# Performance work log

Hardware: AMD Instinct MI355X
Metric: run time of the kernel (lower is better)

Reference implementation:

```python
import jax, jax.numpy as jnp
import numpy as np

NEG_SLOPE = 0.1
BN_EPS = 1e-5

def lrelu(z):
    return jax.nn.leaky_relu(z, NEG_SLOPE)

def conv1d(x, w, b):
    # x: [B,C,L], w: [O,I,K], 'same' padding for K=3
    y = jax.lax.conv_general_dilated(x, w, (1,), [(1, 1)], dimension_numbers=('NCH', 'OIH', 'NCH'))
    return y + b[None, :, None]

def batchnorm_train(x, g, be):
    # training-mode BatchNorm1d over (B, L) per channel; x: [B,C,L]
    m = x.mean(axis=(0, 2), keepdims=True)
    v = x.var(axis=(0, 2), keepdims=True)
    return g[None, :, None] * (x - m) * jax.lax.rsqrt(v + BN_EPS) + be[None, :, None]

def setup_inputs() -> dict:
    key = jax.random.key(0)
    ks = jax.random.split(key, 16)
    L, B, E = 100, 32, 512
    F, K, M, H, DEC = 256, 3, 128, 512, 512
    D = F + 2  # cnn feats + 2 coord dims
    s = 0.02
    inp = {
        'x': jax.random.normal(ks[0], (L, B, E), jnp.float32),
        'h': jax.random.normal(ks[1], (B, H), jnp.float32),
        'cw1': jax.random.normal(ks[2], (F, E, K), jnp.float32) * s,
        'cb1': jnp.zeros((F,), jnp.float32),
        'g1': jnp.ones((F,), jnp.float32), 'be1': jnp.zeros((F,), jnp.float32),
        'cw2': jax.random.normal(ks[3], (F, F, K), jnp.float32) * s,
        'cb2': jnp.zeros((F,), jnp.float32),
        'g2': jnp.ones((F,), jnp.float32), 'be2': jnp.zeros((F,), jnp.float32),
        'cw3': jax.random.normal(ks[4], (F, F, K), jnp.float32) * s,
        'cb3': jnp.zeros((F,), jnp.float32),
        'g3': jnp.ones((F,), jnp.float32), 'be3': jnp.zeros((F,), jnp.float32),
        'cw4': jax.random.normal(ks[5], (F, F, K), jnp.float32) * s,
        'cb4': jnp.zeros((F,), jnp.float32),
        'g4': jnp.ones((F,), jnp.float32), 'be4': jnp.zeros((F,), jnp.float32),
        'W1': jax.random.normal(ks[6], (2 * D + H, M), jnp.float32) * s,
        'b1': jnp.zeros((M,), jnp.float32),
        'W2': jax.random.normal(ks[7], (M, M), jnp.float32) * s,
        'b2': jnp.zeros((M,), jnp.float32),
        'W3': jax.random.normal(ks[8], (M, M), jnp.float32) * s,
        'b3': jnp.zeros((M,), jnp.float32),
        'W4': jax.random.normal(ks[9], (M, M), jnp.float32) * s,
        'b4': jnp.zeros((M,), jnp.float32),
        'F1': jax.random.normal(ks[10], (M, M), jnp.float32) * s,
        'fb1': jnp.zeros((M,), jnp.float32),
        'F2': jax.random.normal(ks[11], (M, DEC), jnp.float32) * s,
        'fb2': jnp.zeros((DEC,), jnp.float32),
    }
    return inp

def reference(x, h, cw1, cb1, g1, be1, cw2, cb2, g2, be2, cw3, cb3, g3, be3,
              cw4, cb4, g4, be4, W1, b1, W2, b2, W3, b3, W4, b4, F1, fb1, F2, fb2):
    # x: [L,B,E] -> [B,E,L]
    xc = jnp.transpose(x, (1, 2, 0))
    for cw, cb, g, be in ((cw1, cb1, g1, be1), (cw2, cb2, g2, be2),
                          (cw3, cb3, g3, be3), (cw4, cb4, g4, be4)):
        xc = batchnorm_train(lrelu(conv1d(xc, cw, cb)), g, be)
    xc = jnp.transpose(xc, (0, 2, 1))  # [B,L,F]
    B, L, _ = xc.shape
    # coordinate tensor: cvt_coord(i, L) = [(i/sqrt(L)-2)/2, (i%sqrt(L)-2)/2]
    i = jnp.arange(L, dtype=jnp.float32)
    sL = jnp.sqrt(jnp.float32(L))
    coord = jnp.stack([(i / sL - 2.0) / 2.0, (jnp.mod(i, sL) - 2.0) / 2.0], axis=-1)
    xf = jnp.concatenate([xc, jnp.broadcast_to(coord, (B, L, 2))], axis=-1)  # [B,L,D]
    D = xf.shape[-1]
    # pair[b,i,j] = [xf[b,j], xf[b,i], h[b]]; split W1 to avoid materializing concat
    Wa, Wb, Wc = W1[:D], W1[D:2 * D], W1[2 * D:]
    A = xf @ Wa                              # contribution of x_j, [B,L,M]
    C = xf @ Wb + (h @ Wc + b1)[:, None, :]  # contribution of x_i and h, [B,L,M]
    g = lrelu(C[:, :, None, :] + A[:, None, :, :])  # [B,L,L,M]
    g = lrelu(g @ W2 + b2)
    g = lrelu(g @ W3 + b3)
    g = lrelu(g @ W4 + b4)
    s = g.sum(axis=(1, 2))  # sum-pool over all L*L pairs -> [B,M]
    out = lrelu(lrelu(s @ F1 + fb1) @ F2 + fb2)  # [B,dec_hid]
    return out
```

## Files before the change

kernel.cpp:

```cpp
#include <hip/hip_runtime.h>
#include <hip/hip_bf16.h>
#include <stdint.h>
#include <stddef.h>

#define NEG 0.1f

typedef __attribute__((ext_vector_type(8))) short short8;
typedef __attribute__((ext_vector_type(16))) float floatx16;

__device__ __forceinline__ unsigned f2bf(float f) {
  union { float f; unsigned u; } v; v.f = f;
  unsigned r = v.u + 0x7FFFu + ((v.u >> 16) & 1u);
  return r >> 16;
}
__device__ __forceinline__ unsigned pk2bf(float a, float b) {
  __hip_bfloat162 hh = __float22bfloat162_rn(make_float2(a, b));
  union { __hip_bfloat162 h; unsigned u; } v; v.h = hh; return v.u;
}
__device__ __forceinline__ float bits2f(unsigned u) {
  union { unsigned u; float f; } v; v.u = u; return v.f;
}


__global__ void k_prep(const float* __restrict__ cw1, const float* __restrict__ cw2,
                       const float* __restrict__ cw3, const float* __restrict__ cw4,
                       unsigned short* __restrict__ wt1, unsigned short* __restrict__ wt2,
                       unsigned short* __restrict__ wt3, unsigned short* __restrict__ wt4,
                       const float* __restrict__ W1, unsigned short* __restrict__ wabf,
                       const float* __restrict__ W2, const float* __restrict__ W3,
                       const float* __restrict__ W4, unsigned short* __restrict__ wmlp,
                       const float* __restrict__ h, float* __restrict__ hc,
                       float* __restrict__ zmem) {
  __shared__ float tile[256];
  int bid = blockIdx.x, tid = threadIdx.x;
  if (bid < 1280) {
    int z = bid;
    int E; const float* cw; unsigned short* wt;
    if (z < 512) { E = 512; cw = cw1; wt = wt1; }
    else {
      int q = (z - 512) >> 8; E = 256;
      cw = (q == 0) ? cw2 : ((q == 1) ? cw3 : cw4);
      wt = (q == 0) ? wt2 : ((q == 1) ? wt3 : wt4);
      z = (z - 512) & 255;
    }
    int NCw = (3 * E) >> 6;
    int idx = z * 256 + tid;
    int f = idx / E, e = idx - f * E;
    const float* s = cw + (size_t)idx * 3;
    int ct = f >> 5, i32 = f & 31;
#pragma unroll
    for (int ks = 0; ks < 3; ++ks) {
      int kcol = ks * E + e;
      int cg = kcol >> 6, kk = (kcol >> 4) & 3, hh = (kcol >> 3) & 1, j = kcol & 7;
      wt[(size_t)((((ct * NCw + cg) * 4 + kk) * 2 + hh) * 32 + i32) * 8 + j] =
          (unsigned short)f2bf(s[ks]);
    }
  } else if (bid < 1304) {
    int tw = bid - 1280;
    int half = tw / 12, rem = tw % 12, dt = rem >> 1, nt = rem & 1;
    int c = tid & 63, rq = tid >> 6;
    int n = half * 128 + nt * 64 + c;
    int ct = n >> 5, i32 = n & 31;
#pragma unroll
    for (int it = 0; it < 16; ++it) {
      int r2 = rq + it * 4;
      int kp = dt * 64 + r2;
      if (kp < 320) {
        float v = (kp < 258) ? W1[(size_t)(half * 258 + kp) * 128 + nt * 64 + c] : 0.f;
        int cg = kp >> 6, kk = (kp >> 4) & 3, hh = (kp >> 3) & 1, j = kp & 7;
        wabf[(size_t)((((ct * 5 + cg) * 4 + kk) * 2 + hh) * 32 + i32) * 8 + j] =
            (unsigned short)f2bf(v);
      }
    }
  } else if (bid < 1496) {
    int i2 = (bid - 1304) * 256 + tid;
    int n = i2 & 127, k = (i2 >> 7) & 127, zz = i2 >> 14;
    const float* W = (zz == 0) ? W2 : ((zz == 1) ? W3 : W4);
    float v = W[k * 128 + n];
    int w = n >> 5, l = ((k >> 3) & 1) * 32 + (n & 31), kk = k >> 4, j = k & 7;
    int i = (((zz * 4 + w) * 8 + kk) << 9) | (l << 3) | j;
    wmlp[i] = (unsigned short)f2bf(v);
  } else if (bid < 1528) {
    int b = bid - 1496;
    int m = tid & 127, kh = tid >> 7;
    const float* hr = h + b * 512 + kh * 256;
    const float* Wc = W1 + (size_t)(516 + kh * 256) * 128 + m;
    float a0 = 0.f, a1 = 0.f, a2 = 0.f, a3 = 0.f, a4 = 0.f, a5 = 0.f, a6 = 0.f, a7 = 0.f;
#pragma unroll
    for (int k = 0; k < 256; k += 8) {
      a0 += hr[k + 0] * Wc[(size_t)(k + 0) * 128];
      a1 += hr[k + 1] * Wc[(size_t)(k + 1) * 128];
      a2 += hr[k + 2] * Wc[(size_t)(k + 2) * 128];
      a3 += hr[k + 3] * Wc[(size_t)(k + 3) * 128];
      a4 += hr[k + 4] * Wc[(size_t)(k + 4) * 128];
      a5 += hr[k + 5] * Wc[(size_t)(k + 5) * 128];
      a6 += hr[k + 6] * Wc[(size_t)(k + 6) * 128];
      a7 += hr[k + 7] * Wc[(size_t)(k + 7) * 128];
    }
    float s = ((a0 + a1) + (a2 + a3)) + ((a4 + a5) + (a6 + a7));
    tile[tid] = s;
    __syncthreads();
    if (kh == 0) hc[b * 128 + m] = tile[m] + tile[128 + m];
  } else {
    int i = (bid - 1528) * 256 + tid;
    zmem[i] = 0.f;
  }
}

__global__ __launch_bounds__(256, 4) void k_conv(
    const float* __restrict__ zin, const float* __restrict__ bnin,
    const float* __restrict__ gamv, const float* __restrict__ betv,
    const unsigned short* __restrict__ wtf, const float* __restrict__ cb,
    float* __restrict__ zout, float* __restrict__ bnout, int E, int xmode) {
  extern __shared__ unsigned short smem[];
  const int SL = (E == 512) ? 520 : 264;
  unsigned short* slab = smem;
  const int NC = (3 * E) >> 6, NCQ = NC >> 2;
  const int esh = (E == 512) ? 9 : 8;
  int tid = threadIdx.x;
  int lane = tid & 63, wave = tid >> 6;
  int bid = blockIdx.x;
  int r0 = (bid % 100) * 32, ct = bid / 100;
  int i32 = lane & 31, h = lane >> 5;

  int lrow = (r0 + i32) % 100;
  bool vks0 = (lrow >= 1), vks2 = (lrow <= 98);

  if (xmode) {
    for (int s = wave; s < 34; s += 4) {
      int m = r0 - 1 + s; m = min(max(m, 0), 3199);
      int b = m / 100, l = m - b * 100;
      size_t base = (size_t)(l * 32 + b) * 512;
#pragma unroll
      for (int cc = 0; cc < 2; ++cc) {
        int ch = cc * 256 + lane * 4;
        float4 v = *(const float4*)(zin + base + ch);
        uint2 p; p.x = pk2bf(v.x, v.y); p.y = pk2bf(v.z, v.w);
        *(uint2*)(&slab[s * SL + ch]) = p;
      }
    }
  } else {
    const float inv = 1.f / 3200.f;
    float sc[4], sh[4];
#pragma unroll
    for (int q = 0; q < 4; ++q) {
      int ch = lane * 4 + q;
      float mme = bnin[ch] * inv;
      float var = bnin[256 + ch] * inv - mme * mme;
      sc[q] = gamv[ch] * rsqrtf(var + 1e-5f);
      sh[q] = betv[ch] - mme * sc[q];
    }
    for (int s = wave; s < 34; s += 4) {
      int m = r0 - 1 + s; m = min(max(m, 0), 3199);
      float4 v = *(const float4*)(zin + (size_t)m * 256 + lane * 4);
      uint2 p;
      p.x = pk2bf(v.x * sc[0] + sh[0], v.y * sc[1] + sh[1]);
      p.y = pk2bf(v.z * sc[2] + sh[2], v.w * sc[3] + sh[3]);
      *(uint2*)(&slab[s * SL + lane * 4]) = p;
    }
  }
  __syncthreads();

  floatx16 acc;
#pragma unroll
  for (int q = 0; q < 16; ++q) acc[q] = 0.f;

  int cg0 = wave * NCQ;
  const unsigned short* wp = wtf + (size_t)((ct * NC + cg0) * 8 + h) * 256 + i32 * 8;
  short8 bpre[4];
#pragma unroll
  for (int kk = 0; kk < 4; ++kk) bpre[kk] = *(const short8*)(wp + kk * 512);

  for (int c = 0; c < NCQ; ++c) {
    short8 bcur[4];
#pragma unroll
    for (int kk = 0; kk < 4; ++kk) bcur[kk] = bpre[kk];
    if (c + 1 < NCQ) {
      wp += 2048;
#pragma unroll
      for (int kk = 0; kk < 4; ++kk) bpre[kk] = *(const short8*)(wp + kk * 512);
    }
    int cg = cg0 + c;
    int ks = (cg << 6) >> esh;
    int ebase = (cg << 6) & (E - 1);
    bool v = (ks == 0) ? vks0 : ((ks == 2) ? vks2 : true);
    int srow = i32 + ks;
#pragma unroll
    for (int kk = 0; kk < 4; ++kk) {
      short8 a = {};
      if (v) a = *(const short8*)(&slab[srow * SL + ebase + kk * 16 + h * 8]);
      acc = __builtin_amdgcn_mfma_f32_32x32x16_bf16(a, bcur[kk], acc, 0, 0, 0);
    }
  }

  __syncthreads();
  float* scr = (float*)smem;
  if (wave) {
#pragma unroll
    for (int reg = 0; reg < 16; ++reg) {
      int rowp = (reg & 3) + 8 * (reg >> 2) + 4 * h;
      scr[(wave - 1) * 1024 + rowp * 32 + i32] = acc[reg];
    }
  }
  __syncthreads();
  if (wave == 0) {
    int f = ct * 32 + i32;
    float bias = cb[f];
    float s1 = 0.f, s2 = 0.f;
#pragma unroll
    for (int reg = 0; reg < 16; ++reg) {
      int rowp = (reg & 3) + 8 * (reg >> 2) + 4 * h;
      int m = r0 + rowp;
      float v = acc[reg] + scr[rowp * 32 + i32] + scr[1024 + rowp * 32 + i32]
              + scr[2048 + rowp * 32 + i32] + bias;
      v = fmaxf(v, NEG * v);
      zout[(size_t)m * 256 + f] = v;
      s1 += v; s2 += v * v;
    }
    s1 += __shfl_xor(s1, 32, 64);
    s2 += __shfl_xor(s2, 32, 64);
    if (lane < 32) { atomicAdd(&bnout[f], s1); atomicAdd(&bnout[256 + f], s2); }
  }
}

__global__ __launch_bounds__(256, 4) void k_ac(
    const float* __restrict__ zin, const float* __restrict__ bnin,
    const float* __restrict__ gamv, const float* __restrict__ betv,
    const unsigned short* __restrict__ wabf, const float* __restrict__ hc,
    const float* __restrict__ b1v,
    unsigned short* __restrict__ Abf, unsigned short* __restrict__ Cbf) {
  extern __shared__ unsigned short smem[];
  unsigned short* slab = smem;
  int tid = threadIdx.x;
  int lane = tid & 63, wave = tid >> 6;
  int bid = blockIdx.x;
  int r0 = (bid % 100) * 32, ct = bid / 100;
  int i32 = lane & 31, h = lane >> 5;
  const float inv = 1.f / 3200.f;

  {
    float sc[4], sh[4];
#pragma unroll
    for (int q = 0; q < 4; ++q) {
      int ch = lane * 4 + q;
      float mme = bnin[ch] * inv;
      float var = bnin[256 + ch] * inv - mme * mme;
      sc[q] = gamv[ch] * rsqrtf(var + 1e-5f);
      sh[q] = betv[ch] - mme * sc[q];
    }
    for (int s = wave; s < 32; s += 4) {
      int m = r0 + s;
      float4 v = *(const float4*)(zin + (size_t)m * 256 + lane * 4);
      uint2 p;
      p.x = pk2bf(v.x * sc[0] + sh[0], v.y * sc[1] + sh[1]);
      p.y = pk2bf(v.z * sc[2] + sh[2], v.w * sc[3] + sh[3]);
      *(uint2*)(&slab[s * 328 + lane * 4]) = p;
    }
    if (wave == 0) {
      int s = i32, half = h * 32;
      int m = r0 + s, l = m % 100;
      float c0 = ((float)l * 0.1f - 2.0f) * 0.5f;
      float c1 = ((float)(l % 10) - 2.0f) * 0.5f;
#pragma unroll
      for (int seg = 0; seg < 4; ++seg) {
        uint4 z4; z4.x = z4.y = z4.z = z4.w = 0u;
        if (half == 0 && seg == 0) z4.x = pk2bf(c0, c1);
        *(uint4*)(&slab[s * 328 + 256 + half + seg * 8]) = z4;
      }
    }
  }
  __syncthreads();

  floatx16 acc;
#pragma unroll
  for (int q = 0; q < 16; ++q) acc[q] = 0.f;

#pragma unroll
  for (int cc = 0; cc < 2; ++cc) {
    int cg = wave + cc * 4;
    if (cg <= 4) {
      const unsigned short* wp = wabf + (size_t)((ct * 5 + cg) * 8 + h) * 256 + i32 * 8;
#pragma unroll
      for (int kk = 0; kk < 4; ++kk) {
        short8 a = *(const short8*)(&slab[i32 * 328 + cg * 64 + kk * 16 + h * 8]);
        short8 b8 = *(const short8*)(wp + kk * 512);
        acc = __builtin_amdgcn_mfma_f32_32x32x16_bf16(a, b8, acc, 0, 0, 0);
      }
    }
  }

  __syncthreads();
  float* scr = (float*)smem;
  if (wave) {
#pragma unroll
    for (int reg = 0; reg < 16; ++reg) {
      int rowp = (reg & 3) + 8 * (reg >> 2) + 4 * h;
      scr[(wave - 1) * 1024 + rowp * 32 + i32] = acc[reg];
    }
  }
  __syncthreads();
  if (wave == 0) {
    int n = ct * 32 + i32;
#pragma unroll
    for (int reg = 0; reg < 16; ++reg) {
      int rowp = (reg & 3) + 8 * (reg >> 2) + 4 * h;
      int m = r0 + rowp;
      float v = acc[reg] + scr[rowp * 32 + i32] + scr[1024 + rowp * 32 + i32]
              + scr[2048 + rowp * 32 + i32];
      if (ct < 4) {
        Abf[(size_t)m * 128 + n] = (unsigned short)f2bf(v);
      } else {
        int b = m / 100;
        int nc = n - 128;
        Cbf[(size_t)m * 128 + nc] =
            (unsigned short)f2bf(v + hc[b * 128 + nc] + b1v[nc]);
      }
    }
  }
}

__device__ __forceinline__ void mlp_layer(const int z, const unsigned short* wlds,
                                          const float* bias_lds, const int lane,
                                          const int h, const short8 (&gin)[8],
                                          short8 (&gout)[8]) {
#pragma unroll
  for (int a = 0; a < 4; ++a) {
    floatx16 acc;
#pragma unroll
    for (int qg = 0; qg < 4; ++qg) {
      float4 bb = *(const float4*)(bias_lds + z * 128 + a * 32 + qg * 8 + h * 4);
      acc[qg * 4 + 0] = bb.x; acc[qg * 4 + 1] = bb.y;
      acc[qg * 4 + 2] = bb.z; acc[qg * 4 + 3] = bb.w;
    }
#pragma unroll
    for (int kk = 0; kk < 8; ++kk) {
      short8 wf = *(const short8*)(wlds + (((z * 4 + a) * 8 + kk) << 9) + lane * 8);
      acc = __builtin_amdgcn_mfma_f32_32x32x16_bf16(wf, gin[kk], acc, 0, 0, 0);
    }
#pragma unroll
    for (int q = 0; q < 16; ++q) {
      float v = acc[q];
      acc[q] = fmaxf(v, NEG * v);
    }
#pragma unroll
    for (int c = 0; c < 2; ++c) {
      unsigned X0 = pk2bf(acc[8 * c + 0], acc[8 * c + 1]);
      unsigned X1 = pk2bf(acc[8 * c + 2], acc[8 * c + 3]);
      unsigned Y0 = pk2bf(acc[8 * c + 4], acc[8 * c + 5]);
      unsigned Y1 = pk2bf(acc[8 * c + 6], acc[8 * c + 7]);
      auto p0 = __builtin_amdgcn_permlane32_swap(X0, Y0, false, false);
      auto p1 = __builtin_amdgcn_permlane32_swap(X1, Y1, false, false);
      union { unsigned w[4]; short8 s; } uu;
      uu.w[0] = (unsigned)p0[0]; uu.w[1] = (unsigned)p1[0];
      uu.w[2] = (unsigned)p0[1]; uu.w[3] = (unsigned)p1[1];
      gout[2 * a + c] = uu.s;
    }
  }
}

__global__ __launch_bounds__(1024, 4) void k_mlp(
    const unsigned short* __restrict__ Abf, const unsigned short* __restrict__ Cbf,
    const unsigned short* __restrict__ wmlp, const float* __restrict__ b2,
    const float* __restrict__ b3, const float* __restrict__ b4,
    float* __restrict__ sout) {
  extern __shared__ unsigned short wsm[];
  float* bias_lds = (float*)(wsm + 49152);
  int tid = threadIdx.x, lane = tid & 63, wave = tid >> 6;
  int ln31 = lane & 31, h = lane >> 5;

  {
    const uint4* s4 = (const uint4*)wmlp;
    uint4* d4 = (uint4*)wsm;
#pragma unroll
    for (int i = 0; i < 6; ++i) d4[tid + i * 1024] = s4[tid + i * 1024];
    if (tid < 256) bias_lds[tid] = (tid < 128) ? b2[tid] : b3[tid - 128];
  }
  float b4v[4];
#pragma unroll
  for (int a = 0; a < 4; ++a) b4v[a] = b4[a * 32 + ln31];
  __syncthreads();

  int slot = blockIdx.x * 16 + wave;
  for (int it = 0; it < 3; ++it) {
    int u = it * 4096 + slot;
    if (u >= 10016) break;
    int b = u / 313, lu = u - b * 313;
    bool tail = (lu == 312);
    int r = lu * 32 + ln31;
    int rc = tail ? min(r, 9999) : r;
    int i = rc / 100, j = rc - i * 100;
    const unsigned short* Crow = Cbf + (size_t)(b * 100 + i) * 128 + h * 8;
    const unsigned short* Arow = Abf + (size_t)(b * 100 + j) * 128 + h * 8;

    short8 ga[8], gb[8];
#pragma unroll
    for (int kk = 0; kk < 8; ++kk) {
      uint4 c4 = *(const uint4*)(Crow + kk * 16);
      uint4 a4 = *(const uint4*)(Arow + kk * 16);
      unsigned cw[4] = {c4.x, c4.y, c4.z, c4.w};
      unsigned aw[4] = {a4.x, a4.y, a4.z, a4.w};
      unsigned ow[4];
#pragma unroll
      for (int q = 0; q < 4; ++q) {
        float x0 = bits2f(cw[q] << 16) + bits2f(aw[q] << 16);
        float x1 = bits2f(cw[q] & 0xFFFF0000u) + bits2f(aw[q] & 0xFFFF0000u);
        x0 = fmaxf(x0, NEG * x0);
        x1 = fmaxf(x1, NEG * x1);
        ow[q] = pk2bf(x0, x1);
      }
      union { unsigned w[4]; short8 s; } uu;
      uu.w[0] = ow[0]; uu.w[1] = ow[1]; uu.w[2] = ow[2]; uu.w[3] = ow[3];
      ga[kk] = uu.s;
    }

    mlp_layer(0, wsm, bias_lds, lane, h, ga, gb);
    mlp_layer(1, wsm, bias_lds, lane, h, gb, ga);

#pragma unroll
    for (int a = 0; a < 4; ++a) {
      floatx16 acc;
      float binit = b4v[a];
#pragma unroll
      for (int q = 0; q < 16; ++q) acc[q] = binit;
#pragma unroll
      for (int kk = 0; kk < 8; ++kk) {
        short8 wf = *(const short8*)(wsm + (((8 + a) * 8 + kk) << 9) + lane * 8);
        acc = __builtin_amdgcn_mfma_f32_32x32x16_bf16(ga[kk], wf, acc, 0, 0, 0);
      }
      float s = 0.f;
      if (!tail) {
#pragma unroll
        for (int reg = 0; reg < 16; ++reg) {
          float v = acc[reg];
          s += fmaxf(v, NEG * v);
        }
      } else {
#pragma unroll
        for (int reg = 0; reg < 16; ++reg) {
          int rowp = (reg & 3) + 8 * (reg >> 2) + 4 * h;
          float v = acc[reg];
          v = fmaxf(v, NEG * v);
          s += (lu * 32 + rowp < 10000) ? v : 0.f;
        }
      }
      s += __shfl_xor(s, 32, 64);
      if (lane < 32) atomicAdd(&sout[b * 128 + a * 32 + ln31], s);
    }
  }
}

__global__ void k_final(const float* __restrict__ s, const float* __restrict__ F1,
                        const float* __restrict__ fb1, const float* __restrict__ F2,
                        const float* __restrict__ fb2, float* __restrict__ out) {
  __shared__ float sl[128], t1[128];
  int b = blockIdx.x, t = threadIdx.x;
  if (t < 128) sl[t] = s[b * 128 + t];
  __syncthreads();
  if (t < 128) {
    float a = fb1[t];
    for (int k = 0; k < 128; ++k) a += sl[k] * F1[k * 128 + t];
    t1[t] = fmaxf(a, NEG * a);
  }
  __syncthreads();
  for (int o = t; o < 512; o += 256) {
    float a = fb2[o];
    for (int k = 0; k < 128; ++k) a += t1[k] * F2[k * 512 + o];
    out[b * 512 + o] = fmaxf(a, NEG * a);
  }
}

extern "C" void kernel_launch(void* const* d_in, const int* in_sizes, int n_in,
                              void* d_out, int out_size, void* d_ws, size_t ws_size,
                              hipStream_t stream) {
  const float* x   = (const float*)d_in[0];
  const float* h   = (const float*)d_in[1];
  const float* cw1 = (const float*)d_in[2];
  const float* cb1 = (const float*)d_in[3];
  const float* g1  = (const float*)d_in[4];
  const float* be1 = (const float*)d_in[5];
  const float* cw2 = (const float*)d_in[6];
  const float* cb2 = (const float*)d_in[7];
  const float* g2  = (const float*)d_in[8];
  const float* be2 = (const float*)d_in[9];
  const float* cw3 = (const float*)d_in[10];
  const float* cb3 = (const float*)d_in[11];
  const float* g3  = (const float*)d_in[12];
  const float* be3 = (const float*)d_in[13];
  const float* cw4 = (const float*)d_in[14];
  const float* cb4 = (const float*)d_in[15];
  const float* g4  = (const float*)d_in[16];
  const float* be4 = (const float*)d_in[17];
  const float* W1  = (const float*)d_in[18];
  const float* b1  = (const float*)d_in[19];
  const float* W2  = (const float*)d_in[20];
  const float* b2  = (const float*)d_in[21];
  const float* W3  = (const float*)d_in[22];
  const float* b3  = (const float*)d_in[23];
  const float* W4  = (const float*)d_in[24];
  const float* b4  = (const float*)d_in[25];
  const float* F1  = (const float*)d_in[26];
  const float* fb1 = (const float*)d_in[27];
  const float* F2  = (const float*)d_in[28];
  const float* fb2 = (const float*)d_in[29];

  char* ws = (char*)d_ws;
  float* zmem = (float*)(ws + 0);
  float* bn0  = (float*)(ws + 0);
  float* bn1  = (float*)(ws + 2048);
  float* bn2  = (float*)(ws + 4096);
  float* bn3  = (float*)(ws + 6144);
  float* sbuf = (float*)(ws + 8192);
  float* hc   = (float*)(ws + 24576);
  float* za   = (float*)(ws + 40960);
  float* zb   = (float*)(ws + 3317760);
  unsigned short* wt1  = (unsigned short*)(ws + 6594560);
  unsigned short* wt2  = (unsigned short*)(ws + 7380992);
  unsigned short* wt3  = (unsigned short*)(ws + 7774208);
  unsigned short* wt4  = (unsigned short*)(ws + 8167424);
  unsigned short* wabf = (unsigned short*)(ws + 8560640);
  unsigned short* wmlp = (unsigned short*)(ws + 8757248);
  unsigned short* Abf  = (unsigned short*)(ws + 8855552);
  unsigned short* Cbf  = (unsigned short*)(ws + 9674752);

  k_prep<<<1552, 256, 0, stream>>>(cw1, cw2, cw3, cw4, wt1, wt2, wt3, wt4,
                                   W1, wabf, W2, W3, W4, wmlp, h, hc, zmem);

  const int lds1 = 34 * 520 * 2;
  const int lds2 = 34 * 264 * 2;
  k_conv<<<800, 256, lds1, stream>>>(x,  nullptr, nullptr, nullptr, wt1, cb1, za, bn0, 512, 1);
  k_conv<<<800, 256, lds2, stream>>>(za, bn0, g1, be1, wt2, cb2, zb, bn1, 256, 0);
  k_conv<<<800, 256, lds2, stream>>>(zb, bn1, g2, be2, wt3, cb3, za, bn2, 256, 0);
  k_conv<<<800, 256, lds2, stream>>>(za, bn2, g3, be3, wt4, cb4, zb, bn3, 256, 0);

  const int ldsa = 32 * 328 * 2;
  k_ac<<<800, 256, ldsa, stream>>>(zb, bn3, g4, be4, wabf, hc, b1, Abf, Cbf);

  const int ldsm = 49152 * 2 + 256 * 4;
  k_mlp<<<256, 1024, ldsm, stream>>>(Abf, Cbf, wmlp, b2, b3, b4, sbuf);
  k_final<<<32, 256, 0, stream>>>(sbuf, F1, fb1, F2, fb2, (float*)d_out);
}
```

Measured before the change: 258.5 us.

## Fuse final MLP into k_mlp via last-block ticket, shrink blocks and LDS

The separate k_final launch is removed. k_mlp now runs a last-block-done pattern: each block bumps a global counter reset in k_prep, and the final block reads the pooled sums and computes the F1/F2 head. k_mlp also moves to 512-thread blocks (512 blocks), with a per-batch slot mapping that drops the division. Only the W2/W3 weights are staged in LDS and W4 fragments are read straight from global, cutting LDS per block to allow more resident blocks. The cost is serial tail work done by one block and extra global loads for W4.

```diff
diff --git a/kernel.cpp b/kernel.cpp
--- a/kernel.cpp
+++ b/kernel.cpp
@@ -30,7 +30,7 @@
                        const float* __restrict__ W2, const float* __restrict__ W3,
                        const float* __restrict__ W4, unsigned short* __restrict__ wmlp,
                        const float* __restrict__ h, float* __restrict__ hc,
-                       float* __restrict__ zmem) {
+                       float* __restrict__ zmem, unsigned* __restrict__ cnt) {
   __shared__ float tile[256];
   int bid = blockIdx.x, tid = threadIdx.x;
   if (bid < 1280) {
@@ -104,6 +104,7 @@
   } else {
     int i = (bid - 1528) * 256 + tid;
     zmem[i] = 0.f;
+    if (bid == 1528 && tid == 0) *cnt = 0u;
   }
 }
 
@@ -358,13 +359,16 @@
   }
 }
 
-__global__ __launch_bounds__(1024, 4) void k_mlp(
+__global__ __launch_bounds__(512, 4) void k_mlp(
     const unsigned short* __restrict__ Abf, const unsigned short* __restrict__ Cbf,
     const unsigned short* __restrict__ wmlp, const float* __restrict__ b2,
     const float* __restrict__ b3, const float* __restrict__ b4,
-    float* __restrict__ sout) {
+    float* __restrict__ sout, unsigned* __restrict__ cnt,
+    const float* __restrict__ F1, const float* __restrict__ fb1,
+    const float* __restrict__ F2, const float* __restrict__ fb2,
+    float* __restrict__ out) {
   extern __shared__ unsigned short wsm[];
-  float* bias_lds = (float*)(wsm + 49152);
+  float* bias_lds = (float*)(wsm + 32768);
   int tid = threadIdx.x, lane = tid & 63, wave = tid >> 6;
   int ln31 = lane & 31, h = lane >> 5;
 
@@ -372,7 +376,7 @@
     const uint4* s4 = (const uint4*)wmlp;
     uint4* d4 = (uint4*)wsm;
 #pragma unroll
-    for (int i = 0; i < 6; ++i) d4[tid + i * 1024] = s4[tid + i * 1024];
+    for (int i = 0; i < 8; ++i) d4[tid + i * 512] = s4[tid + i * 512];
     if (tid < 256) bias_lds[tid] = (tid < 128) ? b2[tid] : b3[tid - 128];
   }
   float b4v[4];
@@ -380,11 +384,12 @@
   for (int a = 0; a < 4; ++a) b4v[a] = b4[a * 32 + ln31];
   __syncthreads();
 
-  int slot = blockIdx.x * 16 + wave;
+  int slot = blockIdx.x * 8 + wave;
+  int b = slot >> 7;
+  int luq = slot & 127;
   for (int it = 0; it < 3; ++it) {
-    int u = it * 4096 + slot;
-    if (u >= 10016) break;
-    int b = u / 313, lu = u - b * 313;
+    int lu = luq + it * 128;
+    if (lu >= 313) break;
     bool tail = (lu == 312);
     int r = lu * 32 + ln31;
     int rc = tail ? min(r, 9999) : r;
@@ -424,7 +429,7 @@
       for (int q = 0; q < 16; ++q) acc[q] = binit;
 #pragma unroll
       for (int kk = 0; kk < 8; ++kk) {
-        short8 wf = *(const short8*)(wsm + (((8 + a) * 8 + kk) << 9) + lane * 8);
+        short8 wf = *(const short8*)(wmlp + (((8 + a) * 8 + kk) << 9) + lane * 8);
         acc = __builtin_amdgcn_mfma_f32_32x32x16_bf16(ga[kk], wf, acc, 0, 0, 0);
       }
       float s = 0.f;
@@ -447,25 +452,49 @@
       if (lane < 32) atomicAdd(&sout[b * 128 + a * 32 + ln31], s);
     }
   }
-}
-
-__global__ void k_final(const float* __restrict__ s, const float* __restrict__ F1,
-                        const float* __restrict__ fb1, const float* __restrict__ F2,
-                        const float* __restrict__ fb2, float* __restrict__ out) {
-  __shared__ float sl[128], t1[128];
-  int b = blockIdx.x, t = threadIdx.x;
-  if (t < 128) sl[t] = s[b * 128 + t];
-  __syncthreads();
-  if (t < 128) {
-    float a = fb1[t];
-    for (int k = 0; k < 128; ++k) a += sl[k] * F1[k * 128 + t];
-    t1[t] = fmaxf(a, NEG * a);
-  }
-  __syncthreads();
-  for (int o = t; o < 512; o += 256) {
-    float a = fb2[o];
-    for (int k = 0; k < 128; ++k) a += t1[k] * F2[k * 512 + o];
-    out[b * 512 + o] = fmaxf(a, NEG * a);
+
+  __syncthreads();
+  unsigned* tickp = (unsigned*)((char*)wsm + 66560);
+  if (tid == 0) {
+    __threadfence();
+    *tickp = atomicAdd(cnt, 1u);
+  }
+  __syncthreads();
+  if (*tickp == 511u) {
+    float* fs  = (float*)wsm;
+    float* fs2 = fs + 4096;
+    for (int i = tid; i < 4096; i += 512)
+      fs[i] = __hip_atomic_load(&sout[i], __ATOMIC_RELAXED, __HIP_MEMORY_SCOPE_AGENT);
+    __syncthreads();
+    for (int ii = tid; ii < 4096; ii += 512) {
+      int bb = ii >> 7, m = ii & 127;
+      const float* ss = fs + bb * 128;
+      const float* Fp = F1 + m;
+      float a0 = 0.f, a1 = 0.f, a2 = 0.f, a3 = 0.f;
+      for (int k = 0; k < 128; k += 4) {
+        a0 += ss[k + 0] * Fp[(size_t)(k + 0) * 128];
+        a1 += ss[k + 1] * Fp[(size_t)(k + 1) * 128];
+        a2 += ss[k + 2] * Fp[(size_t)(k + 2) * 128];
+        a3 += ss[k + 3] * Fp[(size_t)(k + 3) * 128];
+      }
+      float a = fb1[m] + ((a0 + a1) + (a2 + a3));
+      fs2[ii] = fmaxf(a, NEG * a);
+    }
+    __syncthreads();
+    for (int oi = tid; oi < 16384; oi += 512) {
+      int bb = oi >> 9, o = oi & 511;
+      const float* t1p = fs2 + bb * 128;
+      const float* Fp = F2 + o;
+      float a0 = 0.f, a1 = 0.f, a2 = 0.f, a3 = 0.f;
+      for (int k = 0; k < 128; k += 4) {
+        a0 += t1p[k + 0] * Fp[(size_t)(k + 0) * 512];
+        a1 += t1p[k + 1] * Fp[(size_t)(k + 1) * 512];
+        a2 += t1p[k + 2] * Fp[(size_t)(k + 2) * 512];
+        a3 += t1p[k + 3] * Fp[(size_t)(k + 3) * 512];
+      }
+      float a = fb2[o] + ((a0 + a1) + (a2 + a3));
+      out[bb * 512 + o] = fmaxf(a, NEG * a);
+    }
   }
 }
 
@@ -518,12 +547,13 @@
   unsigned short* wt3  = (unsigned short*)(ws + 7774208);
   unsigned short* wt4  = (unsigned short*)(ws + 8167424);
   unsigned short* wabf = (unsigned short*)(ws + 8560640);
+  unsigned* cnt        = (unsigned*)(ws + 8724480);
   unsigned short* wmlp = (unsigned short*)(ws + 8757248);
   unsigned short* Abf  = (unsigned short*)(ws + 8855552);
   unsigned short* Cbf  = (unsigned short*)(ws + 9674752);
 
   k_prep<<<1552, 256, 0, stream>>>(cw1, cw2, cw3, cw4, wt1, wt2, wt3, wt4,
-                                   W1, wabf, W2, W3, W4, wmlp, h, hc, zmem);
+                                   W1, wabf, W2, W3, W4, wmlp, h, hc, zmem, cnt);
 
   const int lds1 = 34 * 520 * 2;
   const int lds2 = 34 * 264 * 2;
@@ -535,7 +565,7 @@
   const int ldsa = 32 * 328 * 2;
   k_ac<<<800, 256, ldsa, stream>>>(zb, bn3, g4, be4, wabf, hc, b1, Abf, Cbf);
 
-  const int ldsm = 49152 * 2 + 256 * 4;
-  k_mlp<<<256, 1024, ldsm, stream>>>(Abf, Cbf, wmlp, b2, b3, b4, sbuf);
-  k_final<<<32, 256, 0, stream>>>(sbuf, F1, fb1, F2, fb2, (float*)d_out);
-}
+  const int ldsm = 32768 * 2 + 256 * 4 + 16;
+  k_mlp<<<512, 512, ldsm, stream>>>(Abf, Cbf, wmlp, b2, b3, b4, sbuf, cnt,
+                                    F1, fb1, F2, fb2, (float*)d_out);
+}
```

New measurement: 555.1 us. 2.15x slower.
